# Optimization experiments

Measured on AMD Instinct MI355X. Metric: run time of the kernel, lower is better.

## Reference

```python
import jax, jax.numpy as jnp
import numpy as np

B, S, HID = 2, 2048, 4096
H, P, N, G, K = 128, 64, 128, 8, 4      # heads, head_dim, ssm_state, groups, conv kernel
INTER = H * P                           # 8192
CONV_DIM = INTER + 2 * G * N            # 10240
CHUNK = 128
EPS = 1e-5
DT_MIN, DT_MAX = 0.0, 100.0


def setup_inputs() -> dict:
    key = jax.random.key(0)
    ks = jax.random.split(key, 4)
    proj = INTER + CONV_DIM + H
    return {
        "x": jax.random.normal(ks[0], (B, S, HID), jnp.float32),
        "in_proj_w": jax.random.normal(ks[1], (proj, HID), jnp.float32) * 0.02,
        "conv_w": jax.random.normal(ks[2], (CONV_DIM, 1, K), jnp.float32) * 0.2,
        "conv_b": jnp.zeros((CONV_DIM,), jnp.float32),
        "dt_bias": jnp.ones((H,), jnp.float32),
        "A_log": jnp.log(jnp.arange(1, H + 1, dtype=jnp.float32)),
        "D": jnp.ones((H,), jnp.float32),
        "norm_w": jnp.ones((INTER,), jnp.float32),
        "out_proj_w": jax.random.normal(ks[3], (HID, INTER), jnp.float32) * 0.02,
    }


def _segsum(a):
    # a: (..., c) -> (..., c, c); [i, j] = sum_{k=j+1..i} a[k] for i >= j, else -inf
    c = a.shape[-1]
    s = jnp.cumsum(a, axis=-1)
    diff = s[..., :, None] - s[..., None, :]
    mask = jnp.tril(jnp.ones((c, c), dtype=bool))
    return jnp.where(mask, diff, -jnp.inf)


def reference(x, in_proj_w, conv_w, conv_b, dt_bias, A_log, D, norm_w, out_proj_w):
    b, s, _ = x.shape
    proj = jnp.einsum('bsd,ed->bse', x, in_proj_w)
    gate = proj[..., :INTER]
    hBC = proj[..., INTER:INTER + CONV_DIM]
    dt = proj[..., INTER + CONV_DIM:]                       # (b, s, H)

    # depthwise causal conv1d + silu
    xc = jnp.transpose(hBC, (0, 2, 1))                      # (b, conv_dim, s)
    xc = jax.lax.conv_general_dilated(xc, conv_w, (1,), [(K - 1, 0)],
                                      dimension_numbers=('NCH', 'OIH', 'NCH'),
                                      feature_group_count=CONV_DIM)
    xc = xc + conv_b[None, :, None]
    hBC = jax.nn.silu(jnp.transpose(xc, (0, 2, 1)))

    hs = hBC[..., :INTER].reshape(b, s, H, P)
    Bm = hBC[..., INTER:INTER + G * N].reshape(b, s, G, N)
    Cm = hBC[..., INTER + G * N:].reshape(b, s, G, N)

    A = -jnp.exp(A_log)                                     # (H,)
    dt = jnp.clip(jax.nn.softplus(dt + dt_bias), DT_MIN, DT_MAX)

    rep = H // G
    Bh = jnp.repeat(Bm, rep, axis=2)                        # (b, s, H, N)
    Ch = jnp.repeat(Cm, rep, axis=2)

    nc = s // CHUNK
    xch = (hs * dt[..., None]).reshape(b, nc, CHUNK, H, P)  # dt-scaled input, chunked
    Bc = Bh.reshape(b, nc, CHUNK, H, N)
    Cc = Ch.reshape(b, nc, CHUNK, H, N)
    A_dt = (dt * A).reshape(b, nc, CHUNK, H).transpose(0, 3, 1, 2)  # (b, H, nc, c)
    A_cum = jnp.cumsum(A_dt, axis=-1)

    # intra-chunk (diagonal) contribution
    L = jnp.exp(_segsum(A_dt))                              # (b, H, nc, c, c)
    Y_diag = jnp.einsum('bzlhn,bzshn,bhzls,bzshp->bzlhp', Cc, Bc, L, xch)

    # per-chunk final states
    decay_states = jnp.exp(A_cum[..., -1:] - A_cum)         # (b, H, nc, c)
    states = jnp.einsum('bzlhn,bhzl,bzlhp->bzhpn', Bc, decay_states, xch)

    # inter-chunk recurrence (initial state = 0)
    states_p = jnp.concatenate([jnp.zeros_like(states[:, :1]), states], axis=1)  # (b, nc+1, H, P, N)
    A_last = jnp.pad(A_cum[..., -1], ((0, 0), (0, 0), (1, 0)))                   # (b, H, nc+1)
    decay_chunk = jnp.exp(_segsum(A_last))                                        # (b, H, nc+1, nc+1)
    new_states = jnp.einsum('bhzc,bchpn->bzhpn', decay_chunk, states_p)
    prev = new_states[:, :-1]                                # state entering each chunk

    Y_off = jnp.einsum('bzlhn,bzhpn,bhzl->bzlhp', Cc, prev, jnp.exp(A_cum))
    Y = (Y_diag + Y_off).reshape(b, s, H, P) + hs * D[None, None, :, None]
    y = Y.reshape(b, s, INTER)

    # gated grouped RMSNorm (norm_before_gate=False)
    g = y * jax.nn.silu(gate)
    gg = g.reshape(b, s, G, INTER // G)
    var = jnp.mean(gg * gg, axis=-1, keepdims=True)
    gg = gg * jax.lax.rsqrt(var + EPS)
    out = gg.reshape(b, s, INTER) * norm_w

    return jnp.einsum('bsi,oi->bso', out, out_proj_w)
```

## Files before the change

### kernel.cpp

```cpp
#include <hip/hip_runtime.h>
#include <hip/hip_bf16.h>
#include <cstdint>
#include <cstddef>

#define DEVI __device__ __forceinline__

#define BB 2
#define S_LEN 2048
#define HID_DIM 4096
#define NH 128
#define PD 64
#define NS 128
#define NG 8
#define INTER 8192
#define CONVD 10240
#define PROJ 18560
#define PROJP 18688
#define NC 16
#define BS 4096
#define GN 1024

using short8 = __attribute__((ext_vector_type(8))) short;
using short4v = __attribute__((ext_vector_type(4))) short;
using f32x4  = __attribute__((ext_vector_type(4))) float;
using bf16x8 = __attribute__((ext_vector_type(8))) __bf16;

DEVI float bf2f(short u) {
  union { unsigned int i; float f; } v;
  v.i = ((unsigned int)(unsigned short)u) << 16;
  return v.f;
}
DEVI short f2bf(float f) {
  union { float ff; unsigned int i; } v; v.ff = f;
  unsigned int x = v.i;
  return (short)((x + 0x7fffu + ((x >> 16) & 1u)) >> 16);
}
DEVI f32x4 mfma16(short8 a, short8 b, f32x4 c) {
  return __builtin_amdgcn_mfma_f32_16x16x32_bf16(
      __builtin_bit_cast(bf16x8, a), __builtin_bit_cast(bf16x8, b), c, 0, 0, 0);
}
DEVI void gl_lds16(const short* g, short* l) {
  __builtin_amdgcn_global_load_lds(
      (const __attribute__((address_space(1))) void*)g,
      (__attribute__((address_space(3))) void*)l, 16, 0, 0);
}
DEVI float sigmoidf_(float x) { return 1.f / (1.f + __expf(-x)); }

__global__ __launch_bounds__(256) void cvt_f32_bf16_k(const float* __restrict__ in,
                                                      short* __restrict__ out, size_t n) {
  size_t i = ((size_t)blockIdx.x * 256 + threadIdx.x) * 8;
  if (i + 8 > n) return;
  float4 a = *(const float4*)(in + i);
  float4 b = *(const float4*)(in + i + 4);
  short8 o;
  o[0] = f2bf(a.x); o[1] = f2bf(a.y); o[2] = f2bf(a.z); o[3] = f2bf(a.w);
  o[4] = f2bf(b.x); o[5] = f2bf(b.y); o[6] = f2bf(b.z); o[7] = f2bf(b.w);
  *(short8*)(out + i) = o;
}

#define STG(ISB, BUF, KH, TILE) do { \
  const short* _src = (ISB) ? Bt : A; \
  const int _r0 = (ISB) ? n0 : m0; \
  short* _lb = lds_ + ((ISB) ? 32768 : 0) + ((BUF)*2+(KH))*8192; \
  const int _kt = (TILE)*64 + (KH)*32; \
  { int _row = (wid*2)*16 + srow; int _sl = sps ^ ((_row>>1)&3); \
    gl_lds16(_src + (size_t)(_r0+_row)*K + _kt + _sl*8, _lb + (wid*2)*512); } \
  { int _row = (wid*2+1)*16 + srow; int _sl = sps ^ ((_row>>1)&3); \
    gl_lds16(_src + (size_t)(_r0+_row)*K + _kt + _sl*8, _lb + (wid*2+1)*512); } \
} while(0)

#define NOPS ((void)0)
#define VM6 asm volatile("s_waitcnt vmcnt(6)" ::: "memory")
#define VM0 asm volatile("s_waitcnt vmcnt(0)" ::: "memory")

#define LDAF(DST, BUF, KH, MIH) do { \
  _Pragma("unroll") \
  for (int _m = 0; _m < 4; ++_m) { \
    int _row = wr*128 + ((MIH)*4+_m)*16 + fr; \
    DST[_m] = *(const short8*)(lds_ + ((BUF)*2+(KH))*8192 + _row*32 + ((slot ^ ((_row>>1)&3))<<3)); \
  } \
} while(0)

#define LDBF(DST, BUF, KH) do { \
  _Pragma("unroll") \
  for (int _n = 0; _n < 4; ++_n) { \
    int _row = wc*64 + _n*16 + fr; \
    DST[_n] = *(const short8*)(lds_ + 32768 + ((BUF)*2+(KH))*8192 + _row*32 + ((slot ^ ((_row>>1)&3))<<3)); \
  } \
} while(0)

#define PH2(CAF, CBF, MIH, PFEN, PFAF, PFBF, PFB, PFKH, PFMIH, PFDOB, STGS, VMW) do { \
  STGS; VMW; \
  __builtin_amdgcn_s_barrier(); \
  if (PFEN) { LDAF(PFAF, PFB, PFKH, PFMIH); if (PFDOB) LDBF(PFBF, PFB, PFKH); } \
  __builtin_amdgcn_s_setprio(1); \
  _Pragma("unroll") \
  for (int _m = 0; _m < 4; ++_m) \
    _Pragma("unroll") \
    for (int _n = 0; _n < 4; ++_n) \
      acc[(MIH)*4+_m][_n] = mfma16(CAF[_m], CBF[_n], acc[(MIH)*4+_m][_n]); \
  __builtin_amdgcn_s_setprio(0); \
  asm volatile("s_waitcnt lgkmcnt(0)" ::: "memory"); \
  __builtin_amdgcn_sched_barrier(0); \
  __builtin_amdgcn_s_barrier(); \
} while(0)

template<int CB16>
__global__ __launch_bounds__(512, 2) void gemm256_k(const short* __restrict__ A,
                                                    const short* __restrict__ Bt,
                                                    void* __restrict__ Cout,
                                                    int Nstride, int K, int ntn) {
  __shared__ short lds_[65536];
  const int tid = threadIdx.x, wid = tid >> 6, lane = tid & 63;
  const int nwg = gridDim.x, orig = blockIdx.x;
  const int swz = (orig & 7) * (nwg >> 3) + (orig >> 3);
  const int per_group = ntn << 3;
  const int group = swz / per_group;
  const int rem = swz - group * per_group;
  const int m0 = (group * 8 + (rem & 7)) * 256;
  const int n0 = (rem >> 3) * 256;
  const int wr = wid >> 2, wc = wid & 3;
  const int fr = lane & 15, slot = lane >> 4;
  const int srow = lane >> 2, sps = lane & 3;

  f32x4 acc[8][4] = {};
  short8 af_a[4], af_b[4], bf_a[4], bf_b[4];
  const int NT = K >> 6;

  STG(1, 0, 0, 0); STG(0, 0, 0, 0); STG(1, 0, 1, 0); STG(0, 0, 1, 0);
  asm volatile("s_waitcnt vmcnt(4)" ::: "memory");
  STG(1, 1, 0, 1); STG(0, 1, 0, 1); STG(1, 1, 1, 1);
  asm volatile("s_waitcnt vmcnt(6)" ::: "memory");
  __builtin_amdgcn_s_barrier();
  LDAF(af_a, 0, 0, 0); LDBF(bf_a, 0, 0);
  asm volatile("s_waitcnt lgkmcnt(0)" ::: "memory");
  __builtin_amdgcn_sched_barrier(0);

  for (int i = 0; i < (NT >> 1) - 1; ++i) {
    const int t = 2 * i;
    PH2(af_a, bf_a, 0, 1, af_b, bf_a, 0, 0, 1, 0, STG(0, 1, 1, t + 1), NOPS);
    PH2(af_b, bf_a, 1, 1, af_a, bf_b, 0, 1, 0, 1, STG(1, 0, 0, t + 2), NOPS);
    PH2(af_a, bf_b, 0, 1, af_b, bf_a, 0, 1, 1, 0, STG(0, 0, 0, t + 2), NOPS);
    PH2(af_b, bf_b, 1, 1, af_a, bf_a, 1, 0, 0, 1, STG(1, 0, 1, t + 2), VM6);
    PH2(af_a, bf_a, 0, 1, af_b, bf_b, 1, 0, 1, 0, STG(0, 0, 1, t + 2), NOPS);
    PH2(af_b, bf_a, 1, 1, af_a, bf_b, 1, 1, 0, 1, STG(1, 1, 0, t + 3), NOPS);
    PH2(af_a, bf_b, 0, 1, af_b, bf_a, 1, 1, 1, 0, STG(0, 1, 0, t + 3), NOPS);
    PH2(af_b, bf_b, 1, 1, af_a, bf_a, 0, 0, 0, 1, STG(1, 1, 1, t + 3), VM6);
  }
  PH2(af_a, bf_a, 0, 1, af_b, bf_a, 0, 0, 1, 0, STG(0, 1, 1, NT - 1), NOPS);
  PH2(af_b, bf_a, 1, 1, af_a, bf_b, 0, 1, 0, 1, NOPS, NOPS);
  PH2(af_a, bf_b, 0, 1, af_b, bf_a, 0, 1, 1, 0, NOPS, NOPS);
  PH2(af_b, bf_b, 1, 1, af_a, bf_a, 1, 0, 0, 1, NOPS, VM0);
  PH2(af_a, bf_a, 0, 1, af_b, bf_b, 1, 0, 1, 0, NOPS, NOPS);
  PH2(af_b, bf_a, 1, 1, af_a, bf_b, 1, 1, 0, 1, NOPS, NOPS);
  PH2(af_a, bf_b, 0, 1, af_b, bf_a, 1, 1, 1, 0, NOPS, NOPS);
  PH2(af_b, bf_b, 1, 0, af_a, bf_a, 0, 0, 0, 0, NOPS, NOPS);

  const int er = (lane >> 4) * 4, ec = lane & 15;
  if (CB16) {
    short* C = (short*)Cout;
#pragma unroll
    for (int mi = 0; mi < 8; ++mi)
#pragma unroll
      for (int j = 0; j < 4; ++j) {
        size_t base = (size_t)(m0 + wr * 128 + mi * 16 + er + j) * Nstride + n0 + wc * 64 + ec;
#pragma unroll
        for (int ni = 0; ni < 4; ++ni) C[base + ni * 16] = f2bf(acc[mi][ni][j]);
      }
  } else {
    float* C = (float*)Cout;
#pragma unroll
    for (int mi = 0; mi < 8; ++mi)
#pragma unroll
      for (int j = 0; j < 4; ++j) {
        size_t base = (size_t)(m0 + wr * 128 + mi * 16 + er + j) * Nstride + n0 + wc * 64 + ec;
#pragma unroll
        for (int ni = 0; ni < 4; ++ni) C[base + ni * 16] = acc[mi][ni][j];
      }
  }
}

__global__ __launch_bounds__(256) void conv_silu_k(const short* __restrict__ projb,
                                                   const float* __restrict__ convw,
                                                   const float* __restrict__ convb,
                                                   short* __restrict__ hbc) {
  const int c = blockIdx.x * 256 + threadIdx.x;
  const int s0 = blockIdx.y * 256;
  const int b = blockIdx.z;
  const size_t rb = (size_t)b * S_LEN;
  const float* wp = convw + (size_t)c * 4;
  const float w0 = wp[0], w1 = wp[1], w2 = wp[2], w3 = wp[3];
  const float bias = convb[c];
  const short* pcol = projb + INTER + c;
  float x1 = 0.f, x2 = 0.f, x3 = 0.f;
  if (s0 > 0) {
    x3 = bf2f(pcol[(rb + s0 - 3) * PROJP]);
    x2 = bf2f(pcol[(rb + s0 - 2) * PROJP]);
    x1 = bf2f(pcol[(rb + s0 - 1) * PROJP]);
  }
  for (int s = s0; s < s0 + 256; ++s) {
    float v = bf2f(pcol[(rb + s) * PROJP]);
    float acc = bias + w0 * x3 + w1 * x2 + w2 * x1 + w3 * v;
    float o = acc * sigmoidf_(acc);
    hbc[(rb + s) * CONVD + c] = f2bf(o);
    x3 = x2; x2 = x1; x1 = v;
  }
}

__global__ __launch_bounds__(128) void acum_k(const short* __restrict__ projb,
                                              const float* __restrict__ dt_bias,
                                              const float* __restrict__ A_log,
                                              float* __restrict__ dtT,
                                              float* __restrict__ acum) {
  const int l = threadIdx.x;
  const int z = blockIdx.x, h = blockIdx.y, b = blockIdx.z;
  const float A = -__expf(A_log[h]);
  __shared__ float sv[128];
  const int r = b * S_LEN + z * 128 + l;
  float xv = bf2f(projb[(size_t)r * PROJP + INTER + CONVD + h]) + dt_bias[h];
  float sp = (xv > 20.f) ? xv : log1pf(__expf(xv));
  sp = fminf(fmaxf(sp, 0.f), 100.f);
  const size_t base = ((size_t)(b * NH + h)) * S_LEN + z * 128;
  dtT[base + l] = sp;
  sv[l] = sp * A;
  __syncthreads();
  for (int off = 1; off < 128; off <<= 1) {
    float t = (l >= off) ? sv[l - off] : 0.f;
    __syncthreads();
    sv[l] += t;
    __syncthreads();
  }
  acum[base + l] = sv[l];
}

__global__ __launch_bounds__(512) void states_k(const short* __restrict__ hbc,
                                                const float* __restrict__ dtT,
                                                const float* __restrict__ acum,
                                                float* __restrict__ states) {
  __shared__ short sBT[128 * 136];
  __shared__ short sxdt2[2][64 * 136];
  const int tid = threadIdx.x, wid = tid >> 6, lane = tid & 63;
  const int g = blockIdx.x, z = blockIdx.y, b = blockIdx.z;
  const size_t srow0 = (size_t)(b * S_LEN + z * 128);
  const short* hrow = hbc + srow0 * CONVD;

  {
    const int l = tid & 127, n0b = (tid >> 7) * 32;
    const short* src = hrow + (size_t)l * CONVD + INTER + g * NS + n0b;
    short8 v0 = *(const short8*)(src);
    short8 v1 = *(const short8*)(src + 8);
    short8 v2 = *(const short8*)(src + 16);
    short8 v3 = *(const short8*)(src + 24);
#pragma unroll
    for (int j = 0; j < 8; ++j) {
      sBT[(n0b + j) * 136 + l] = v0[j];
      sBT[(n0b + 8 + j) * 136 + l] = v1[j];
      sBT[(n0b + 16 + j) * 136 + l] = v2[j];
      sBT[(n0b + 24 + j) * 136 + l] = v3[j];
    }
  }

  const int fr = lane & 15, fk8 = (lane >> 4) * 8;
  const int er = (lane >> 4) * 4, ec = lane & 15;
  const int pband = (wid & 3) * 16, nhalf = (wid >> 2) * 64;
  const int s2 = tid & 63, p0w = (tid >> 6) * 8;

  float cdv0, cdv1; short8 cr0, cr1;
  {
    const int h = g * 16;
    const float* acg = acum + ((size_t)(b * NH + h)) * S_LEN + z * 128;
    const float* dts = dtT + ((size_t)(b * NH + h)) * S_LEN + z * 128;
    const float acL = acg[127];
    cdv0 = dts[2 * s2] * __expf(acL - acg[2 * s2]);
    cdv1 = dts[2 * s2 + 1] * __expf(acL - acg[2 * s2 + 1]);
    const short* rsrc = hrow + (size_t)(2 * s2) * CONVD + (size_t)h * PD + p0w;
    cr0 = *(const short8*)(rsrc);
    cr1 = *(const short8*)(rsrc + CONVD);
  }
  {
    unsigned int* x32 = (unsigned int*)sxdt2[0];
#pragma unroll
    for (int j = 0; j < 8; ++j) {
      unsigned int lo = (unsigned short)f2bf(bf2f(cr0[j]) * cdv0);
      unsigned int hi = (unsigned short)f2bf(bf2f(cr1[j]) * cdv1);
      x32[(p0w + j) * 68 + s2] = lo | (hi << 16);
    }
  }
  __syncthreads();

  for (int hh = 0; hh < 16; ++hh) {
    const int h = g * 16 + hh;
    float ndv0 = 0.f, ndv1 = 0.f; short8 nr0, nr1;
    if (hh < 15) {
      const int h2 = h + 1;
      const float* acg = acum + ((size_t)(b * NH + h2)) * S_LEN + z * 128;
      const float* dts = dtT + ((size_t)(b * NH + h2)) * S_LEN + z * 128;
      const float acL = acg[127];
      ndv0 = dts[2 * s2] * __expf(acL - acg[2 * s2]);
      ndv1 = dts[2 * s2 + 1] * __expf(acL - acg[2 * s2 + 1]);
      const short* rsrc = hrow + (size_t)(2 * s2) * CONVD + (size_t)h2 * PD + p0w;
      nr0 = *(const short8*)(rsrc);
      nr1 = *(const short8*)(rsrc + CONVD);
    }
    const short* sx = sxdt2[hh & 1];
    f32x4 st[4] = {};
#pragma unroll
    for (int kk = 0; kk < 4; ++kk) {
      short8 a = *(const short8*)(sx + (pband + fr) * 136 + kk * 32 + fk8);
#pragma unroll
      for (int ni = 0; ni < 4; ++ni) {
        short8 bb = *(const short8*)(sBT + (nhalf + ni * 16 + fr) * 136 + kk * 32 + fk8);
        st[ni] = mfma16(a, bb, st[ni]);
      }
    }
    float* stp = states + (((size_t)(b * NC + z)) * NH + h) * (size_t)(NS * PD);
#pragma unroll
    for (int ni = 0; ni < 4; ++ni)
#pragma unroll
      for (int j = 0; j < 4; ++j)
        stp[(pband + er + j) * NS + nhalf + ni * 16 + ec] = st[ni][j];
    if (hh < 15) {
      unsigned int* x32 = (unsigned int*)sxdt2[(hh + 1) & 1];
#pragma unroll
      for (int j = 0; j < 8; ++j) {
        unsigned int lo = (unsigned short)f2bf(bf2f(nr0[j]) * ndv0);
        unsigned int hi = (unsigned short)f2bf(bf2f(nr1[j]) * ndv1);
        x32[(p0w + j) * 68 + s2] = lo | (hi << 16);
      }
    }
    __syncthreads();
  }
}

__global__ __launch_bounds__(256) void scan_k(float* __restrict__ states,
                                              const float* __restrict__ acum) {
  const int h = blockIdx.x, b = blockIdx.y;
  const int tid = threadIdx.x;
  float* stp = states + ((size_t)(b * NC * NH) + h) * (size_t)(NS * PD);
  const size_t cst = (size_t)NH * NS * PD;
  const float* ac = acum + ((size_t)(b * NH + h)) * S_LEN;
  float E[32];
#pragma unroll
  for (int i = 0; i < 32; ++i) E[i] = 0.f;
  const int n = tid & 127, pg = tid >> 7;
  for (int zz = 0; zz < NC; ++zz) {
    float* sz = stp + (size_t)zz * cst;
    short* pvb = (short*)sz;
    float tmp[32];
#pragma unroll
    for (int i = 0; i < 32; ++i) tmp[i] = sz[i * 256 + tid];
    __syncthreads();
    float dec = __expf(ac[zz * 128 + 127]);
#pragma unroll
    for (int i = 0; i < 32; ++i) {
      int p = i * 2 + pg;
      pvb[p * 128 + n] = f2bf(E[i]);
      E[i] = dec * E[i] + tmp[i];
    }
    __syncthreads();
  }
}

#define RDSW(BUF, ROWBASE, KK) \
  (*(const short8*)((BUF) + ((ROWBASE) + fr) * 128 + ((((KK) * 4 + slot4) ^ sw7) << 3)))

#define WRX(DST, D0, D1, R0, R1) do { \
  unsigned int* _x = (unsigned int*)(DST); \
  _Pragma("unroll") \
  for (int _j = 0; _j < 8; ++_j) { \
    unsigned int _lo = (unsigned short)f2bf(bf2f(R0[_j]) * (D0)); \
    unsigned int _hi = (unsigned short)f2bf(bf2f(R1[_j]) * (D1)); \
    _x[(p0w + _j) * 64 + ((((s2 >> 2) ^ _j) << 2) | (s2 & 3))] = _lo | (_hi << 16); \
  } \
} while (0)

#define WRP(DST, P0, P1) do { \
  int _p = tid >> 3; int _s0 = (tid & 7) * 2; int _m = _p & 7; \
  *(short8*)((DST) + _p * 128 + ((_s0 ^ _m) << 3)) = P0; \
  *(short8*)((DST) + _p * 128 + (((_s0 + 1) ^ _m) << 3)) = P1; \
} while (0)

#define LOADH_Y(H, DT0, DT1, ACS, ACL, R0, R1, P0, P1) do { \
  const float* _ac = acum + ((size_t)(b * NH + (H))) * S_LEN + z * 128; \
  const float* _dts = dtT + ((size_t)(b * NH + (H))) * S_LEN + z * 128; \
  DT0 = _dts[2 * s2]; DT1 = _dts[2 * s2 + 1]; \
  _Pragma("unroll") \
  for (int _si = 0; _si < 8; ++_si) ACS[_si] = _ac[_si * 16 + ec]; \
  _Pragma("unroll") \
  for (int _j = 0; _j < 4; ++_j) ACL[_j] = _ac[lrow + er + _j]; \
  const short* _rs = hrow + (size_t)(2 * s2) * CONVD + (size_t)(H) * PD + p0w; \
  R0 = *(const short8*)(_rs); R1 = *(const short8*)(_rs + CONVD); \
  const short* _pv = (const short*)(states + (((size_t)(b * NC + z)) * NH + (H)) * (size_t)(NS * PD)); \
  P0 = *(const short8*)(_pv + tid * 16); P1 = *(const short8*)(_pv + tid * 16 + 8); \
} while (0)

__global__ __launch_bounds__(512) void yfull_k(const short* __restrict__ hbc,
                                               const short* __restrict__ projb,
                                               const float* __restrict__ dtT,
                                               const float* __restrict__ acum,
                                               const float* __restrict__ states,
                                               const float* __restrict__ Dv,
                                               const float* __restrict__ norm_w,
                                               short* __restrict__ normed) {
  __shared__ short lds[66560];
  __shared__ float sScale[128];
  __shared__ float sNW[1024];
  short* sC = lds;
  short* sB = lds + 16384;
  short* sx0 = lds + 32768;
  short* sp0 = lds + 40960;
  const int tid = threadIdx.x, wid = tid >> 6, lane = tid & 63;
  short* sPw = lds + 49152 + wid * 2176;
  const int g = blockIdx.x, z = blockIdx.y, b = blockIdx.z;
  const size_t srow0 = (size_t)(b * S_LEN + z * 128);
  const short* hrow = hbc + srow0 * CONVD;

  {
    const int slot_g = (lane & 15) ^ (((wid & 1) << 2) | (lane >> 4));
    const int n0_ = slot_g * 8;
#pragma unroll
    for (int it = 0; it < 4; ++it) {
      int s = it * 32 + wid * 4 + (lane >> 4);
      gl_lds16(hrow + (size_t)s * CONVD + INTER + GN + g * NS + n0_, sC + (it * 32 + wid * 4) * 128);
      gl_lds16(hrow + (size_t)s * CONVD + INTER + g * NS + n0_, sB + (it * 32 + wid * 4) * 128);
    }
  }
  for (int i = tid; i < 1024; i += 512) sNW[i] = norm_w[g * 1024 + i];
  __syncthreads();

  const int fr = lane & 15, fk8 = (lane >> 4) * 8;
  const int slot4 = lane >> 4, sw7 = lane & 7;
  const int er = (lane >> 4) * 4, ec = lane & 15;
  const int lrow = wid * 16;
  const int s2 = tid & 63, p0w = (tid >> 6) * 8;

  float cdt0, cdt1, cacS[8], cacl[4];
  short8 cr0, cr1, cp0, cp1;
  LOADH_Y(g * 16, cdt0, cdt1, cacS, cacl, cr0, cr1, cp0, cp1);

  f32x4 sc[8] = {};
#pragma unroll
  for (int kk = 0; kk < 4; ++kk) {
    short8 a = RDSW(sC, lrow, kk);
#pragma unroll
    for (int si = 0; si < 8; ++si) {
      short8 bv = RDSW(sB, si * 16, kk);
      sc[si] = mfma16(a, bv, sc[si]);
    }
  }
  WRX(sx0, cdt0, cdt1, cr0, cr1);
  WRP(sp0, cp0, cp1);
  __syncthreads();

  float rssq[4] = {0.f, 0.f, 0.f, 0.f};

  for (int hh = 0; hh < 16; ++hh) {
    const int h = g * 16 + hh;
    float ndt0 = 0.f, ndt1 = 0.f, nacS[8], nacl[4];
    short8 nr0, nr1, np0, np1;
    if (hh < 15) LOADH_Y(h + 1, ndt0, ndt1, nacS, nacl, nr0, nr1, np0, np1);

    short* sx = (hh & 1) ? sB : sx0;
    short* sp = (hh & 1) ? (sB + 8192) : sp0;

#pragma unroll
    for (int j = 0; j < 4; ++j) {
      int lloc = er + j;
      float acl = cacl[j];
#pragma unroll
      for (int si = 0; si < 8; ++si) {
        int sI = si * 16 + ec;
        float v = (sI <= lrow + lloc) ? sc[si][j] * __expf(acl - cacS[si]) : 0.f;
        sPw[lloc * 136 + sI] = f2bf(v);
      }
    }
    f32x4 yd[4] = {}, yo[4] = {};
#pragma unroll
    for (int kk = 0; kk < 4; ++kk) {
      short8 ap = *(const short8*)(sPw + fr * 136 + kk * 32 + fk8);
      short8 acf = RDSW(sC, lrow, kk);
#pragma unroll
      for (int ni = 0; ni < 4; ++ni) {
        short8 bv = RDSW(sx, ni * 16, kk);
        yd[ni] = mfma16(ap, bv, yd[ni]);
        short8 bp = RDSW(sp, ni * 16, kk);
        yo[ni] = mfma16(acf, bp, yo[ni]);
      }
    }
    const float Dh = Dv[h];
#pragma unroll
    for (int j = 0; j < 4; ++j) {
      int l = lrow + er + j;
      float e_ac = __expf(cacl[j]);
#pragma unroll
      for (int ni = 0; ni < 4; ++ni) {
        int p = ni * 16 + ec;
        float hs = bf2f(hrow[(size_t)l * CONVD + (size_t)h * PD + p]);
        float y = yd[ni][j] + yo[ni][j] * e_ac + hs * Dh;
        float gate = bf2f(projb[(srow0 + l) * (size_t)PROJP + (size_t)h * PD + p]);
        float gg = y * gate * sigmoidf_(gate);
        normed[(srow0 + l) * (size_t)INTER + (size_t)h * PD + p] = f2bf(gg);
        rssq[j] += gg * gg;
      }
    }
    if (hh < 15) {
      short* nx = (hh & 1) ? sx0 : sB;
      short* npv = (hh & 1) ? sp0 : (sB + 8192);
      WRX(nx, ndt0, ndt1, nr0, nr1);
      WRP(npv, np0, np1);
      cdt0 = ndt0; cdt1 = ndt1; cr0 = nr0; cr1 = nr1; cp0 = np0; cp1 = np1;
#pragma unroll
      for (int si = 0; si < 8; ++si) cacS[si] = nacS[si];
#pragma unroll
      for (int j = 0; j < 4; ++j) cacl[j] = nacl[j];
    }
    __syncthreads();
  }

#pragma unroll
  for (int j = 0; j < 4; ++j) {
#pragma unroll
    for (int m = 1; m <= 8; m <<= 1) rssq[j] += __shfl_xor(rssq[j], m, 64);
  }
  if (ec == 0) {
#pragma unroll
    for (int j = 0; j < 4; ++j) sScale[lrow + er + j] = rsqrtf(rssq[j] * (1.f / 1024.f) + 1e-5f);
  }
  __syncthreads();

  for (int e = tid * 8; e < 128 * 1024; e += 4096) {
    int row = e >> 10, ch = e & 1023;
    short* gp = normed + (srow0 + row) * (size_t)INTER + g * 1024 + ch;
    short8 gv = *(const short8*)(gp);
    float scl = sScale[row];
    short8 o;
#pragma unroll
    for (int q = 0; q < 8; ++q) o[q] = f2bf(bf2f(gv[q]) * scl * sNW[ch + q]);
    *(short8*)(gp) = o;
  }
}

extern "C" void kernel_launch(void* const* d_in, const int* in_sizes, int n_in,
                              void* d_out, int out_size, void* d_ws, size_t ws_size,
                              hipStream_t stream) {
  const float* x     = (const float*)d_in[0];
  const float* w1    = (const float*)d_in[1];
  const float* convw = (const float*)d_in[2];
  const float* convb = (const float*)d_in[3];
  const float* dtb   = (const float*)d_in[4];
  const float* alog  = (const float*)d_in[5];
  const float* Dv    = (const float*)d_in[6];
  const float* nw    = (const float*)d_in[7];
  const float* w2    = (const float*)d_in[8];
  float* out = (float*)d_out;

  char* ws = (char*)d_ws;
  size_t off = 0;
  float* dtT = (float*)(ws + off);  off += (size_t)BB * NH * S_LEN * 4;
  float* acum = (float*)(ws + off); off += (size_t)BB * NH * S_LEN * 4;
  short* xb = (short*)(ws + off);   off += (size_t)BS * HID_DIM * 2;
  char* w1region = ws + off;        off += (size_t)PROJP * HID_DIM * 2;
  short* w1b = (short*)w1region;
  short* normed = (short*)w1region;
  short* w2b = (short*)(w1region + (size_t)BS * INTER * 2);
  short* projb = (short*)(ws + off); off += (size_t)BS * PROJP * 2;
  short* hbc = (short*)(ws + off);   off += (size_t)BS * CONVD * 2;
  float* states = (float*)(ws + off); off += (size_t)BB * NC * NH * NS * PD * 4;

  const size_t nx = (size_t)BS * HID_DIM;
  const size_t nw1 = (size_t)PROJ * HID_DIM;
  const size_t nw2 = (size_t)HID_DIM * INTER;

  cvt_f32_bf16_k<<<dim3(nx / 2048), 256, 0, stream>>>(x, xb, nx);
  cvt_f32_bf16_k<<<dim3(nw1 / 2048), 256, 0, stream>>>(w1, w1b, nw1);

  gemm256_k<1><<<dim3(16 * 73), 512, 0, stream>>>(xb, w1b, projb, PROJP, HID_DIM, 73);

  cvt_f32_bf16_k<<<dim3(nw2 / 2048), 256, 0, stream>>>(w2, w2b, nw2);

  conv_silu_k<<<dim3(CONVD / 256, S_LEN / 256, BB), 256, 0, stream>>>(projb, convw, convb, hbc);
  acum_k<<<dim3(NC, NH, BB), 128, 0, stream>>>(projb, dtb, alog, dtT, acum);

  states_k<<<dim3(NG, NC, BB), 512, 0, stream>>>(hbc, dtT, acum, states);
  scan_k<<<dim3(NH, BB), 256, 0, stream>>>(states, acum);
  yfull_k<<<dim3(NG, NC, BB), 512, 0, stream>>>(hbc, projb, dtT, acum, states, Dv, nw, normed);

  gemm256_k<0><<<dim3(16 * 16), 512, 0, stream>>>(normed, w2b, out, HID_DIM, INTER, 16);
}
```

Baseline: 1.183 ms.

## Replace 8-phase ping-pong GEMM schedule with simpler 2-stage per-tile pipeline

Restructures the main loop of the 256x256 bf16 GEMM kernel. The finely interleaved 8-phase ping-pong schedule, with staggered half-tile global->LDS loads and fragment prefetch, becomes a per-K-tile iteration: issue the next tile's loads into the other buffer, wait, barrier, read both K-halves' fragments, and run two MFMA batches. It removes sched_barriers and cuts barriers per tile, aiming for simpler, less synchronization-heavy code. The cost is less overlap of LDS reads with MFMA work, and loads are waited on more tightly.

```diff
diff --git a/kernel.cpp b/kernel.cpp
--- a/kernel.cpp
+++ b/kernel.cpp
@@ -58,6 +58,7 @@
   *(short8*)(out + i) = o;
 }
 
+
 #define STG(ISB, BUF, KH, TILE) do { \
   const short* _src = (ISB) ? Bt : A; \
   const int _r0 = (ISB) ? n0 : m0; \
@@ -69,8 +70,7 @@
     gl_lds16(_src + (size_t)(_r0+_row)*K + _kt + _sl*8, _lb + (wid*2+1)*512); } \
 } while(0)
 
-#define NOPS ((void)0)
-#define VM6 asm volatile("s_waitcnt vmcnt(6)" ::: "memory")
+#define VM4 asm volatile("s_waitcnt vmcnt(4)" ::: "memory")
 #define VM0 asm volatile("s_waitcnt vmcnt(0)" ::: "memory")
 
 #define LDAF(DST, BUF, KH, MIH) do { \
@@ -89,19 +89,31 @@
   } \
 } while(0)
 
-#define PH2(CAF, CBF, MIH, PFEN, PFAF, PFBF, PFB, PFKH, PFMIH, PFDOB, STGS, VMW) do { \
-  STGS; VMW; \
-  __builtin_amdgcn_s_barrier(); \
-  if (PFEN) { LDAF(PFAF, PFB, PFKH, PFMIH); if (PFDOB) LDBF(PFBF, PFB, PFKH); } \
-  __builtin_amdgcn_s_setprio(1); \
+#define MFMA16X(MIH, AF, BF) do { \
   _Pragma("unroll") \
   for (int _m = 0; _m < 4; ++_m) \
     _Pragma("unroll") \
     for (int _n = 0; _n < 4; ++_n) \
-      acc[(MIH)*4+_m][_n] = mfma16(CAF[_m], CBF[_n], acc[(MIH)*4+_m][_n]); \
+      acc[(MIH)*4+_m][_n] = mfma16(AF[_m], BF[_n], acc[(MIH)*4+_m][_n]); \
+} while(0)
+
+#define ITER(CB, NB, TNEXT, DOSTG, VMW) do { \
+  if (DOSTG) { STG(0, NB, 0, TNEXT); STG(1, NB, 0, TNEXT); } \
+  VMW; \
+  __builtin_amdgcn_s_barrier(); \
+  LDAF(af0, CB, 0, 0); LDAF(af1, CB, 1, 0); \
+  LDBF(bf0, CB, 0); LDBF(bf1, CB, 1); \
+  __builtin_amdgcn_s_setprio(1); \
+  MFMA16X(0, af0, bf0); \
+  MFMA16X(0, af1, bf1); \
+  __builtin_amdgcn_s_setprio(0); \
+  if (DOSTG) { STG(0, NB, 1, TNEXT); STG(1, NB, 1, TNEXT); } \
+  LDAF(af0, CB, 0, 1); LDAF(af1, CB, 1, 1); \
+  __builtin_amdgcn_s_setprio(1); \
+  MFMA16X(1, af0, bf0); \
+  MFMA16X(1, af1, bf1); \
   __builtin_amdgcn_s_setprio(0); \
   asm volatile("s_waitcnt lgkmcnt(0)" ::: "memory"); \
-  __builtin_amdgcn_sched_barrier(0); \
   __builtin_amdgcn_s_barrier(); \
 } while(0)
 
@@ -124,37 +136,18 @@
   const int srow = lane >> 2, sps = lane & 3;
 
   f32x4 acc[8][4] = {};
-  short8 af_a[4], af_b[4], bf_a[4], bf_b[4];
+  short8 af0[4], af1[4], bf0[4], bf1[4];
   const int NT = K >> 6;
 
-  STG(1, 0, 0, 0); STG(0, 0, 0, 0); STG(1, 0, 1, 0); STG(0, 0, 1, 0);
-  asm volatile("s_waitcnt vmcnt(4)" ::: "memory");
-  STG(1, 1, 0, 1); STG(0, 1, 0, 1); STG(1, 1, 1, 1);
-  asm volatile("s_waitcnt vmcnt(6)" ::: "memory");
-  __builtin_amdgcn_s_barrier();
-  LDAF(af_a, 0, 0, 0); LDBF(bf_a, 0, 0);
-  asm volatile("s_waitcnt lgkmcnt(0)" ::: "memory");
-  __builtin_amdgcn_sched_barrier(0);
-
-  for (int i = 0; i < (NT >> 1) - 1; ++i) {
-    const int t = 2 * i;
-    PH2(af_a, bf_a, 0, 1, af_b, bf_a, 0, 0, 1, 0, STG(0, 1, 1, t + 1), NOPS);
-    PH2(af_b, bf_a, 1, 1, af_a, bf_b, 0, 1, 0, 1, STG(1, 0, 0, t + 2), NOPS);
-    PH2(af_a, bf_b, 0, 1, af_b, bf_a, 0, 1, 1, 0, STG(0, 0, 0, t + 2), NOPS);
-    PH2(af_b, bf_b, 1, 1, af_a, bf_a, 1, 0, 0, 1, STG(1, 0, 1, t + 2), VM6);
-    PH2(af_a, bf_a, 0, 1, af_b, bf_b, 1, 0, 1, 0, STG(0, 0, 1, t + 2), NOPS);
-    PH2(af_b, bf_a, 1, 1, af_a, bf_b, 1, 1, 0, 1, STG(1, 1, 0, t + 3), NOPS);
-    PH2(af_a, bf_b, 0, 1, af_b, bf_a, 1, 1, 1, 0, STG(0, 1, 0, t + 3), NOPS);
-    PH2(af_b, bf_b, 1, 1, af_a, bf_a, 0, 0, 0, 1, STG(1, 1, 1, t + 3), VM6);
-  }
-  PH2(af_a, bf_a, 0, 1, af_b, bf_a, 0, 0, 1, 0, STG(0, 1, 1, NT - 1), NOPS);
-  PH2(af_b, bf_a, 1, 1, af_a, bf_b, 0, 1, 0, 1, NOPS, NOPS);
-  PH2(af_a, bf_b, 0, 1, af_b, bf_a, 0, 1, 1, 0, NOPS, NOPS);
-  PH2(af_b, bf_b, 1, 1, af_a, bf_a, 1, 0, 0, 1, NOPS, VM0);
-  PH2(af_a, bf_a, 0, 1, af_b, bf_b, 1, 0, 1, 0, NOPS, NOPS);
-  PH2(af_b, bf_a, 1, 1, af_a, bf_b, 1, 1, 0, 1, NOPS, NOPS);
-  PH2(af_a, bf_b, 0, 1, af_b, bf_a, 1, 1, 1, 0, NOPS, NOPS);
-  PH2(af_b, bf_b, 1, 0, af_a, bf_a, 0, 0, 0, 0, NOPS, NOPS);
+  STG(0, 0, 0, 0); STG(1, 0, 0, 0); STG(0, 0, 1, 0); STG(1, 0, 1, 0);
+
+  for (int ii = 0; ii < (NT >> 1) - 1; ++ii) {
+    const int t = 2 * ii;
+    ITER(0, 1, t + 1, 1, VM4);
+    ITER(1, 0, t + 2, 1, VM4);
+  }
+  ITER(0, 1, NT - 1, 1, VM4);
+  ITER(1, 0, 0, 0, VM0);
 
   const int er = (lane >> 4) * 4, ec = lane & 15;
   if (CB16) {
```

Measured after the change: 1.172 ms. About the same (-0.9%).
